# Optimization experiments

Hardware: AMD Instinct MI355X
Metric: run time of the kernel (lower is better)

The kernel has to match this reference:

```python
import jax, jax.numpy as jnp
import numpy as np

HIDDEN = 1024
N_HEAD = 16
HEAD_DIM = HIDDEN // N_HEAD


def setup_inputs() -> dict:
    key = jax.random.key(0)
    ks = jax.random.split(key, 11)
    B, S, D, H, E = 4, 1024, HIDDEN, N_HEAD, HEAD_DIM
    sc = 0.02
    return {
        "query": jax.random.normal(ks[0], (B, S, D), jnp.float32),
        "key": jax.random.normal(ks[1], (B, S, D), jnp.float32),
        "value": jax.random.normal(ks[2], (B, S, D), jnp.float32),
        # per-head projection weights stacked over heads (torch Linear: y = x @ W.T + b)
        "Wq": jax.random.normal(ks[3], (H, D, E), jnp.float32) * sc,
        "bq": jax.random.normal(ks[4], (H, E), jnp.float32) * sc,
        "Wk": jax.random.normal(ks[5], (H, D, E), jnp.float32) * sc,
        "bk": jax.random.normal(ks[6], (H, E), jnp.float32) * sc,
        "Wv": jax.random.normal(ks[7], (H, D, E), jnp.float32) * sc,
        "bv": jax.random.normal(ks[8], (H, E), jnp.float32) * sc,
        "Wo": jax.random.normal(ks[9], (D, D), jnp.float32) * sc,
        "bo": jax.random.normal(ks[10], (D,), jnp.float32) * sc,
    }


def reference(query, key, value, Wq, bq, Wk, bk, Wv, bv, Wo, bo):
    B, S, D = query.shape
    H, _, E = Wq.shape
    # per-head linear projections (vectorized over heads)
    q = jnp.einsum("bsd,hde->bhse", query, Wq) + bq[None, :, None, :]
    k = jnp.einsum("bsd,hde->bhse", key, Wk) + bk[None, :, None, :]
    v = jnp.einsum("bsd,hde->bhse", value, Wv) + bv[None, :, None, :]
    scale = jnp.sqrt(jnp.asarray(E, q.dtype))
    scores = jnp.einsum("bhse,bhte->bhst", q, k) / scale  # [B,H,S,S]
    attn = jax.nn.softmax(scores, axis=-1)  # dropout is identity in eval
    wv = jnp.einsum("bhst,bhte->bhse", attn, v)  # [B,H,S,E]
    # concat heads along feature dim (head h -> slice h*E:(h+1)*E)
    wv = wv.transpose(0, 2, 1, 3).reshape(B, S, H * E)
    out = wv @ Wo.T + bo  # final linear; output dropout identity in eval
    return out
```

## Files before the change

### kernel.cpp

```cpp
#include <hip/hip_runtime.h>

typedef unsigned short u16;
typedef unsigned int u32;
typedef __attribute__((ext_vector_type(8))) short bf16x8;
typedef __attribute__((ext_vector_type(4))) float f32x4;

#define B_SZ 4
#define S_SZ 1024
#define D_SZ 1024
#define H_SZ 16
#define E_SZ 64
#define M_SZ (B_SZ * S_SZ)

__device__ __forceinline__ u16 f2bf(float f) {
  union { float f; unsigned u; } x; x.f = f;
  unsigned r = (x.u + 0x7FFFu + ((x.u >> 16) & 1u)) >> 16;
  return (u16)r;
}

__device__ __forceinline__ u32 pack_bf16(float lo, float hi) {
  return (u32)f2bf(lo) | ((u32)f2bf(hi) << 16);
}

__device__ __forceinline__ void async16(const void* g, void* l) {
  __builtin_amdgcn_global_load_lds(
      (const __attribute__((address_space(1))) void*)g,
      (__attribute__((address_space(3))) void*)l, 16, 0, 0);
}

__device__ __forceinline__ f32x4 mfma16(bf16x8 a, bf16x8 b, f32x4 c) {
  return __builtin_amdgcn_mfma_f32_16x16x32_bf16(a, b, c, 0, 0, 0);
}

__global__ void cast4(const float* __restrict__ q, const float* __restrict__ k,
                      const float* __restrict__ v, const float* __restrict__ Wo,
                      u16* __restrict__ oq, u16* __restrict__ ok,
                      u16* __restrict__ ov, u16* __restrict__ oWo) {
  int gid = blockIdx.x * 256 + threadIdx.x;
  const float* in;
  u16* out;
  int i;
  if (gid < (3 << 19)) {
    int sel = gid >> 19;
    i = (gid & ((1 << 19) - 1)) << 3;
    in = sel == 0 ? q : (sel == 1 ? k : v);
    out = sel == 0 ? oq : (sel == 1 ? ok : ov);
  } else {
    i = (gid - (3 << 19)) << 3;
    in = Wo;
    out = oWo;
  }
  float4 a = *(const float4*)(in + i);
  float4 b = *(const float4*)(in + i + 4);
  alignas(16) u16 r[8];
  r[0] = f2bf(a.x); r[1] = f2bf(a.y); r[2] = f2bf(a.z); r[3] = f2bf(a.w);
  r[4] = f2bf(b.x); r[5] = f2bf(b.y); r[6] = f2bf(b.z); r[7] = f2bf(b.w);
  *(uint4*)(out + i) = *(uint4*)r;
}

__global__ void transW3(const float* __restrict__ Wq, const float* __restrict__ Wk,
                        const float* __restrict__ Wv, u16* __restrict__ Tq,
                        u16* __restrict__ Tk, u16* __restrict__ Tv) {
  __shared__ float tile[64 * 68];
  const int wsel = blockIdx.x >> 8;
  const int bi = blockIdx.x & 255;
  const float* W = wsel == 0 ? Wq : (wsel == 1 ? Wk : Wv);
  u16* WT = wsel == 0 ? Tq : (wsel == 1 ? Tk : Tv);
  const int tid = threadIdx.x;
  const int h = bi >> 4;
  const int d0 = (bi & 15) << 6;
#pragma unroll
  for (int c = 0; c < 4; ++c) {
    const int dd = c * 16 + (tid >> 4);
    const int e4 = (tid & 15) << 2;
    float4 vq = *(const float4*)(W + (h << 16) + ((d0 + dd) << 6) + e4);
    *(float4*)(tile + dd * 68 + e4) = vq;
  }
  __syncthreads();
  {
    const int e = tid >> 2;
    const int dc = (tid & 3) << 4;
    alignas(16) u16 outv[16];
#pragma unroll
    for (int i = 0; i < 16; ++i) outv[i] = f2bf(tile[(dc + i) * 68 + e]);
    u16* dst = WT + (((size_t)(h << 6) + e) << 10) + d0 + dc;
    *(uint4*)(dst) = *(uint4*)outv;
    *(uint4*)(dst + 8) = *(uint4*)(outv + 8);
  }
}

__global__ __launch_bounds__(256)
void gemm3(const u16* __restrict__ qb, const u16* __restrict__ kb, const u16* __restrict__ vb,
           const u16* __restrict__ Tq, const u16* __restrict__ Tk, const u16* __restrict__ Tv,
           const float* __restrict__ bq, const float* __restrict__ bk, const float* __restrict__ bv,
           u16* __restrict__ Qp, u16* __restrict__ Kp, u16* __restrict__ VpT) {
  __shared__ u16 Al[128 * 64];
  __shared__ u16 Bl[128 * 64];
  const int wg = blockIdx.x;
  const int swz = (wg & 7) * 96 + (wg >> 3);
  const int g = swz >> 8;
  const int bi = swz & 255;
  const u16* A = g == 0 ? qb : (g == 1 ? kb : vb);
  const u16* BT = g == 0 ? Tq : (g == 1 ? Tk : Tv);
  const float* bias = g == 0 ? bq : (g == 1 ? bk : bv);
  u16* Cout = g == 0 ? Qp : (g == 1 ? Kp : VpT);
  const float scale = g == 0 ? 0.125f : 1.0f;

  const int tid = threadIdx.x;
  const int wave = tid >> 6;
  const int lane = tid & 63;
  const int l15 = lane & 15, lq = lane >> 4;
  const int bm = bi >> 3;
  const int bn = bi & 7;
  const int row0 = bm << 7, col0 = bn << 7;
  const int wr = ((wave >> 1) & 1) << 6;
  const int wc = (wave & 1) << 6;

  f32x4 acc[4][4];
#pragma unroll
  for (int m = 0; m < 4; ++m)
#pragma unroll
    for (int n = 0; n < 4; ++n) acc[m][n] = (f32x4)0.0f;

  for (int k0 = 0; k0 < 1024; k0 += 64) {
    __syncthreads();
#pragma unroll
    for (int c = 0; c < 4; ++c) {
      const int x = c * 4096 + tid * 16;
      const int gx = x ^ (((x >> 7) & 7) << 4);
      const int row = gx >> 7;
      const int cb = gx & 127;
      const u16* ga = A + (size_t)(row0 + row) * 1024 + k0 + (cb >> 1);
      const u16* gb = BT + (size_t)(col0 + row) * 1024 + k0 + (cb >> 1);
      async16(ga, (char*)Al + x);
      async16(gb, (char*)Bl + x);
    }
    __syncthreads();

    bf16x8 af[4][2], bfr[4][2];
#pragma unroll
    for (int m = 0; m < 4; ++m)
#pragma unroll
      for (int kf = 0; kf < 2; ++kf) {
        int r = wr + m * 16 + l15;
        int byte = ((r << 7) + kf * 64 + lq * 16) ^ ((r & 7) << 4);
        af[m][kf] = *(const bf16x8*)((const char*)Al + byte);
      }
#pragma unroll
    for (int n = 0; n < 4; ++n)
#pragma unroll
      for (int kf = 0; kf < 2; ++kf) {
        int r = wc + n * 16 + l15;
        int byte = ((r << 7) + kf * 64 + lq * 16) ^ ((r & 7) << 4);
        bfr[n][kf] = *(const bf16x8*)((const char*)Bl + byte);
      }
    if (g == 2) {
#pragma unroll
      for (int kf = 0; kf < 2; ++kf)
#pragma unroll
        for (int m = 0; m < 4; ++m)
#pragma unroll
          for (int n = 0; n < 4; ++n)
            acc[m][n] = mfma16(af[m][kf], bfr[n][kf], acc[m][n]);
    } else {
#pragma unroll
      for (int kf = 0; kf < 2; ++kf)
#pragma unroll
        for (int m = 0; m < 4; ++m)
#pragma unroll
          for (int n = 0; n < 4; ++n)
            acc[m][n] = mfma16(bfr[n][kf], af[m][kf], acc[m][n]);
    }
  }

  if (g == 2) {
#pragma unroll
    for (int m = 0; m < 4; ++m)
#pragma unroll
      for (int n = 0; n < 4; ++n) {
        int col = col0 + wc + n * 16 + l15;
        float bv = bias[col];
        int rowb = row0 + wr + m * 16 + lq * 4;
        alignas(8) u16 r4[4];
#pragma unroll
        for (int j = 0; j < 4; ++j) r4[j] = f2bf(acc[m][n][j] + bv);
        *(uint2*)(Cout + (size_t)col * 4096 + rowb) = *(uint2*)r4;
      }
  } else {
    float4 b4[4];
#pragma unroll
    for (int n = 0; n < 4; ++n)
      b4[n] = *(const float4*)(bias + col0 + wc + n * 16 + lq * 4);
#pragma unroll
    for (int m = 0; m < 4; ++m) {
      int row = row0 + wr + m * 16 + l15;
#pragma unroll
      for (int n = 0; n < 4; ++n) {
        int colbase = col0 + wc + n * 16 + lq * 4;
        u32 lo = pack_bf16((acc[m][n][0] + b4[n].x) * scale,
                           (acc[m][n][1] + b4[n].y) * scale);
        u32 hi = pack_bf16((acc[m][n][2] + b4[n].z) * scale,
                           (acc[m][n][3] + b4[n].w) * scale);
        uint2 wv; wv.x = lo; wv.y = hi;
        *(uint2*)(Cout + (size_t)row * 1024 + colbase) = wv;
      }
    }
  }
}

__global__ __launch_bounds__(512)
void gemmO8(const u16* __restrict__ A, const u16* __restrict__ BT,
            const float* __restrict__ bias, float* __restrict__ out) {
  __shared__ u16 Al[128 * 64];
  __shared__ u16 Bl[128 * 64];
  const int tid = threadIdx.x;
  const int wave = tid >> 6;
  const int lane = tid & 63;
  const int l15 = lane & 15, lq = lane >> 4;
  const int wg = blockIdx.x;
  const int bi = (wg & 7) * 32 + (wg >> 3);
  const int bm = bi >> 3;
  const int bn = bi & 7;
  const int row0 = bm << 7, col0 = bn << 7;
  const int wr = (wave >> 1) << 5;
  const int wc = (wave & 1) << 6;

  f32x4 acc[2][4];
#pragma unroll
  for (int m = 0; m < 2; ++m)
#pragma unroll
    for (int n = 0; n < 4; ++n) acc[m][n] = (f32x4)0.0f;

  for (int k0 = 0; k0 < 1024; k0 += 64) {
    __syncthreads();
#pragma unroll
    for (int c = 0; c < 2; ++c) {
      const int x = c * 8192 + tid * 16;
      const int gx = x ^ (((x >> 7) & 7) << 4);
      const int row = gx >> 7;
      const int cb = gx & 127;
      const u16* ga = A + (size_t)(row0 + row) * 1024 + k0 + (cb >> 1);
      const u16* gb = BT + (size_t)(col0 + row) * 1024 + k0 + (cb >> 1);
      async16(ga, (char*)Al + x);
      async16(gb, (char*)Bl + x);
    }
    __syncthreads();

    bf16x8 af[2][2], bfr[4][2];
#pragma unroll
    for (int m = 0; m < 2; ++m)
#pragma unroll
      for (int kf = 0; kf < 2; ++kf) {
        int r = wr + m * 16 + l15;
        int byte = ((r << 7) + kf * 64 + lq * 16) ^ ((r & 7) << 4);
        af[m][kf] = *(const bf16x8*)((const char*)Al + byte);
      }
#pragma unroll
    for (int n = 0; n < 4; ++n)
#pragma unroll
      for (int kf = 0; kf < 2; ++kf) {
        int r = wc + n * 16 + l15;
        int byte = ((r << 7) + kf * 64 + lq * 16) ^ ((r & 7) << 4);
        bfr[n][kf] = *(const bf16x8*)((const char*)Bl + byte);
      }
#pragma unroll
    for (int kf = 0; kf < 2; ++kf)
#pragma unroll
      for (int m = 0; m < 2; ++m)
#pragma unroll
        for (int n = 0; n < 4; ++n)
          acc[m][n] = mfma16(bfr[n][kf], af[m][kf], acc[m][n]);
  }

  float4 b4[4];
#pragma unroll
  for (int n = 0; n < 4; ++n)
    b4[n] = *(const float4*)(bias + col0 + wc + n * 16 + lq * 4);
#pragma unroll
  for (int m = 0; m < 2; ++m) {
    int row = row0 + wr + m * 16 + l15;
#pragma unroll
    for (int n = 0; n < 4; ++n) {
      int colbase = col0 + wc + n * 16 + lq * 4;
      float4 v;
      v.x = acc[m][n][0] + b4[n].x;
      v.y = acc[m][n][1] + b4[n].y;
      v.z = acc[m][n][2] + b4[n].z;
      v.w = acc[m][n][3] + b4[n].w;
      *(float4*)(out + (size_t)row * 1024 + colbase) = v;
    }
  }
}

__global__ __launch_bounds__(256)
void attn(const u16* __restrict__ Qp, const u16* __restrict__ Kp,
          const u16* __restrict__ VpT, u16* __restrict__ Ow) {
  __shared__ alignas(16) u16 Kl[2][64 * 64];
  __shared__ alignas(16) u16 VTl[2][64 * 64];
  __shared__ alignas(16) u16 Pl[4][16 * 64];
  const int tid = threadIdx.x;
  const int wave = tid >> 6;
  const int lane = tid & 63;
  const int l15 = lane & 15, lq = lane >> 4;
  const int wg = blockIdx.x;
  const int swz = (wg & 7) * 128 + (wg >> 3);
  const int qt = swz & 15;
  const int bh = swz >> 4;
  const int b = bh >> 4, h = bh & 15;
  const size_t bS = (size_t)b * S_SZ;

  const int xs0 = tid * 16, xs1 = 4096 + tid * 16;
  const int r0 = xs0 >> 7, r1 = xs1 >> 7;
  const int c0 = ((xs0 & 127) ^ (((xs0 >> 7) & 7) << 4)) >> 1;
  const int c1 = ((xs1 & 127) ^ (((xs1 >> 7) & 7) << 4)) >> 1;
  const u16* Kb0 = Kp + ((bS + r0) << 10) + h * 64 + c0;
  const u16* Kb1 = Kp + ((bS + r1) << 10) + h * 64 + c1;
  const u16* Vb0 = VpT + (size_t)(h * 64 + r0) * 4096 + bS + c0;
  const u16* Vb1 = VpT + (size_t)(h * 64 + r1) * 4096 + bS + c1;

  bf16x8 aq[2];
  {
    const u16* qptr = Qp + ((bS + qt * 64 + wave * 16 + l15) << 10) + h * 64 + lq * 8;
    aq[0] = *(const bf16x8*)(qptr);
    aq[1] = *(const bf16x8*)(qptr + 32);
  }

  f32x4 o[4];
#pragma unroll
  for (int n = 0; n < 4; ++n) o[n] = (f32x4)0.0f;
  float m_run = -1e30f;
  float l_run = 0.f;
  u16* Pw = Pl[wave];

  async16(Kb0, (char*)Kl[0] + xs0);
  async16(Kb1, (char*)Kl[0] + xs1);
  async16(Vb0, (char*)VTl[0] + xs0);
  async16(Vb1, (char*)VTl[0] + xs1);
  __syncthreads();

  int buf = 0;
  for (int t0 = 0; t0 < S_SZ; t0 += 64) {
    if (t0 + 64 < S_SZ) {
      const int tn = t0 + 64;
      async16(Kb0 + ((size_t)tn << 10), (char*)Kl[buf ^ 1] + xs0);
      async16(Kb1 + ((size_t)tn << 10), (char*)Kl[buf ^ 1] + xs1);
      async16(Vb0 + tn, (char*)VTl[buf ^ 1] + xs0);
      async16(Vb1 + tn, (char*)VTl[buf ^ 1] + xs1);
    }

    f32x4 s[4];
#pragma unroll
    for (int n = 0; n < 4; ++n) s[n] = (f32x4)0.0f;
    __builtin_amdgcn_s_setprio(1);
#pragma unroll
    for (int n = 0; n < 4; ++n)
#pragma unroll
      for (int kf = 0; kf < 2; ++kf) {
        int r = n * 16 + l15;
        int byte = ((r << 7) + kf * 64 + lq * 16) ^ ((r & 7) << 4);
        bf16x8 bk = *(const bf16x8*)((const char*)Kl[buf] + byte);
        s[n] = mfma16(bk, aq[kf], s[n]);
      }
    __builtin_amdgcn_s_setprio(0);

    float mx = s[0][0];
#pragma unroll
    for (int n = 0; n < 4; ++n)
#pragma unroll
      for (int j = 0; j < 4; ++j) mx = fmaxf(mx, s[n][j]);
    mx = fmaxf(mx, __shfl_xor(mx, 16, 64));
    mx = fmaxf(mx, __shfl_xor(mx, 32, 64));

    if (__any(mx > m_run + 8.0f)) {
      float mn = fmaxf(m_run, mx);
      float alpha = __expf(m_run - mn);
      m_run = mn;
      l_run *= alpha;
      float a0 = __shfl(alpha, lq * 4 + 0, 64);
      float a1 = __shfl(alpha, lq * 4 + 1, 64);
      float a2 = __shfl(alpha, lq * 4 + 2, 64);
      float a3 = __shfl(alpha, lq * 4 + 3, 64);
#pragma unroll
      for (int n = 0; n < 4; ++n) {
        o[n][0] *= a0; o[n][1] *= a1; o[n][2] *= a2; o[n][3] *= a3;
      }
    }

    float rs = 0.f;
#pragma unroll
    for (int n = 0; n < 4; ++n) {
      float p0 = __expf(s[n][0] - m_run);
      float p1 = __expf(s[n][1] - m_run);
      float p2 = __expf(s[n][2] - m_run);
      float p3 = __expf(s[n][3] - m_run);
      rs += (p0 + p1) + (p2 + p3);
      u32 lo = pack_bf16(p0, p1);
      u32 hi = pack_bf16(p2, p3);
      int byte = (l15 << 7) + (((n * 32 + lq * 8)) ^ ((l15 & 7) << 4));
      uint2 wv; wv.x = lo; wv.y = hi;
      *(uint2*)((char*)Pw + byte) = wv;
    }
    rs += __shfl_xor(rs, 16, 64);
    rs += __shfl_xor(rs, 32, 64);
    l_run += rs;

    __builtin_amdgcn_s_setprio(1);
#pragma unroll
    for (int kf = 0; kf < 2; ++kf) {
      int pbyte = (l15 << 7) + ((kf * 64 + lq * 16) ^ ((l15 & 7) << 4));
      bf16x8 pa = *(const bf16x8*)((const char*)Pw + pbyte);
#pragma unroll
      for (int n = 0; n < 4; ++n) {
        int vr = n * 16 + l15;
        int byte = ((vr << 7) + kf * 64 + lq * 16) ^ ((vr & 7) << 4);
        bf16x8 bv = *(const bf16x8*)((const char*)VTl[buf] + byte);
        o[n] = mfma16(pa, bv, o[n]);
      }
    }
    __builtin_amdgcn_s_setprio(0);

    __syncthreads();
    buf ^= 1;
  }

  float li0 = __shfl(l_run, lq * 4 + 0, 64);
  float li1 = __shfl(l_run, lq * 4 + 1, 64);
  float li2 = __shfl(l_run, lq * 4 + 2, 64);
  float li3 = __shfl(l_run, lq * 4 + 3, 64);
  float inv0 = 1.0f / li0, inv1 = 1.0f / li1, inv2 = 1.0f / li2, inv3 = 1.0f / li3;
#pragma unroll
  for (int n = 0; n < 4; ++n) {
    float vals[4] = {o[n][0] * inv0, o[n][1] * inv1, o[n][2] * inv2, o[n][3] * inv3};
#pragma unroll
    for (int j = 0; j < 4; ++j) {
      int row = qt * 64 + wave * 16 + lq * 4 + j;
      int col = h * 64 + n * 16 + l15;
      Ow[((bS + row) << 10) + col] = f2bf(vals[j]);
    }
  }
}

extern "C" void kernel_launch(void* const* d_in, const int* in_sizes, int n_in,
                              void* d_out, int out_size, void* d_ws, size_t ws_size,
                              hipStream_t stream) {
  const float* q  = (const float*)d_in[0];
  const float* k  = (const float*)d_in[1];
  const float* v  = (const float*)d_in[2];
  const float* Wq = (const float*)d_in[3];
  const float* bq = (const float*)d_in[4];
  const float* Wk = (const float*)d_in[5];
  const float* bk = (const float*)d_in[6];
  const float* Wv = (const float*)d_in[7];
  const float* bv = (const float*)d_in[8];
  const float* Wo = (const float*)d_in[9];
  const float* bo = (const float*)d_in[10];

  char* w = (char*)d_ws;
  const size_t MB = 1u << 20;
  u16* qb  = (u16*)(w + 0 * MB);
  u16* kb  = (u16*)(w + 8 * MB);
  u16* vb  = (u16*)(w + 16 * MB);
  u16* WqT = (u16*)(w + 24 * MB);
  u16* WkT = (u16*)(w + 26 * MB);
  u16* WvT = (u16*)(w + 28 * MB);
  u16* Wob = (u16*)(w + 30 * MB);
  u16* Qp  = (u16*)(w + 32 * MB);
  u16* Kp  = (u16*)(w + 40 * MB);
  u16* VpT = (u16*)(w + 48 * MB);
  u16* wvb = (u16*)(w + 56 * MB);

  cast4<<<6656, 256, 0, stream>>>(q, k, v, Wo, qb, kb, vb, Wob);
  transW3<<<768, 256, 0, stream>>>(Wq, Wk, Wv, WqT, WkT, WvT);

  gemm3<<<768, 256, 0, stream>>>(qb, kb, vb, WqT, WkT, WvT, bq, bk, bv, Qp, Kp, VpT);

  attn<<<B_SZ * H_SZ * (S_SZ / 64), 256, 0, stream>>>(Qp, Kp, VpT, wvb);

  gemmO8<<<256, 512, 0, stream>>>(wvb, Wob, bo, (float*)d_out);
}
```

Before: 122.4 us.

## Double-buffer LDS tiles in projection GEMMs and widen gemm3 to 512 threads

Both the QKV projection GEMM and the output GEMM now use two LDS buffers per operand. The next K-slice is prefetched before computing the current one, and only one barrier is issued per iteration instead of two. gemm3 also goes from 4 to 8 waves per block, each wave owning a 32x64 sub-tile, to raise wave-level parallelism. The risks are that the 4-blocks-per-CU launch bound can force register limits low enough to spill, and that the doubled LDS footprint lowers how many blocks fit per CU.

Measured after the change: 128.9 us. 5.3% more time.

```diff
diff --git a/kernel.cpp b/kernel.cpp
--- a/kernel.cpp
+++ b/kernel.cpp
@@ -89,13 +89,13 @@
   }
 }
 
-__global__ __launch_bounds__(256)
+__global__ __launch_bounds__(512, 4)
 void gemm3(const u16* __restrict__ qb, const u16* __restrict__ kb, const u16* __restrict__ vb,
            const u16* __restrict__ Tq, const u16* __restrict__ Tk, const u16* __restrict__ Tv,
            const float* __restrict__ bq, const float* __restrict__ bk, const float* __restrict__ bv,
            u16* __restrict__ Qp, u16* __restrict__ Kp, u16* __restrict__ VpT) {
-  __shared__ u16 Al[128 * 64];
-  __shared__ u16 Bl[128 * 64];
+  __shared__ u16 Al[2][128 * 64];
+  __shared__ u16 Bl[2][128 * 64];
   const int wg = blockIdx.x;
   const int swz = (wg & 7) * 96 + (wg >> 3);
   const int g = swz >> 8;
@@ -113,38 +113,51 @@
   const int bm = bi >> 3;
   const int bn = bi & 7;
   const int row0 = bm << 7, col0 = bn << 7;
-  const int wr = ((wave >> 1) & 1) << 6;
+  const int wr = (wave >> 1) << 5;
   const int wc = (wave & 1) << 6;
 
-  f32x4 acc[4][4];
-#pragma unroll
-  for (int m = 0; m < 4; ++m)
+  int xs[2], rowS[2], cbS[2];
+#pragma unroll
+  for (int c = 0; c < 2; ++c) {
+    int x = c * 8192 + tid * 16;
+    int gx = x ^ (((x >> 7) & 7) << 4);
+    xs[c] = x;
+    rowS[c] = gx >> 7;
+    cbS[c] = (gx & 127) >> 1;
+  }
+
+  f32x4 acc[2][4];
+#pragma unroll
+  for (int m = 0; m < 2; ++m)
 #pragma unroll
     for (int n = 0; n < 4; ++n) acc[m][n] = (f32x4)0.0f;
 
+#pragma unroll
+  for (int c = 0; c < 2; ++c) {
+    async16(A + (size_t)(row0 + rowS[c]) * 1024 + cbS[c], (char*)Al[0] + xs[c]);
+    async16(BT + (size_t)(col0 + rowS[c]) * 1024 + cbS[c], (char*)Bl[0] + xs[c]);
+  }
+  __syncthreads();
+
+  int buf = 0;
   for (int k0 = 0; k0 < 1024; k0 += 64) {
-    __syncthreads();
-#pragma unroll
-    for (int c = 0; c < 4; ++c) {
-      const int x = c * 4096 + tid * 16;
-      const int gx = x ^ (((x >> 7) & 7) << 4);
-      const int row = gx >> 7;
-      const int cb = gx & 127;
-      const u16* ga = A + (size_t)(row0 + row) * 1024 + k0 + (cb >> 1);
-      const u16* gb = BT + (size_t)(col0 + row) * 1024 + k0 + (cb >> 1);
-      async16(ga, (char*)Al + x);
-      async16(gb, (char*)Bl + x);
-    }
-    __syncthreads();
-
-    bf16x8 af[4][2], bfr[4][2];
-#pragma unroll
-    for (int m = 0; m < 4; ++m)
+    if (k0 + 64 < 1024) {
+      const int kn = k0 + 64;
+#pragma unroll
+      for (int c = 0; c < 2; ++c) {
+        async16(A + (size_t)(row0 + rowS[c]) * 1024 + kn + cbS[c], (char*)Al[buf ^ 1] + xs[c]);
+        async16(BT + (size_t)(col0 + rowS[c]) * 1024 + kn + cbS[c], (char*)Bl[buf ^ 1] + xs[c]);
+      }
+    }
+
+    bf16x8 af[2][2], bfr[4][2];
+#pragma unroll
+    for (int m = 0; m < 2; ++m)
 #pragma unroll
       for (int kf = 0; kf < 2; ++kf) {
         int r = wr + m * 16 + l15;
         int byte = ((r << 7) + kf * 64 + lq * 16) ^ ((r & 7) << 4);
-        af[m][kf] = *(const bf16x8*)((const char*)Al + byte);
+        af[m][kf] = *(const bf16x8*)((const char*)Al[buf] + byte);
       }
 #pragma unroll
     for (int n = 0; n < 4; ++n)
@@ -152,13 +165,13 @@
       for (int kf = 0; kf < 2; ++kf) {
         int r = wc + n * 16 + l15;
         int byte = ((r << 7) + kf * 64 + lq * 16) ^ ((r & 7) << 4);
-        bfr[n][kf] = *(const bf16x8*)((const char*)Bl + byte);
+        bfr[n][kf] = *(const bf16x8*)((const char*)Bl[buf] + byte);
       }
     if (g == 2) {
 #pragma unroll
       for (int kf = 0; kf < 2; ++kf)
 #pragma unroll
-        for (int m = 0; m < 4; ++m)
+        for (int m = 0; m < 2; ++m)
 #pragma unroll
           for (int n = 0; n < 4; ++n)
             acc[m][n] = mfma16(af[m][kf], bfr[n][kf], acc[m][n]);
@@ -166,16 +179,19 @@
 #pragma unroll
       for (int kf = 0; kf < 2; ++kf)
 #pragma unroll
-        for (int m = 0; m < 4; ++m)
+        for (int m = 0; m < 2; ++m)
 #pragma unroll
           for (int n = 0; n < 4; ++n)
             acc[m][n] = mfma16(bfr[n][kf], af[m][kf], acc[m][n]);
     }
+
+    __syncthreads();
+    buf ^= 1;
   }
 
   if (g == 2) {
 #pragma unroll
-    for (int m = 0; m < 4; ++m)
+    for (int m = 0; m < 2; ++m)
 #pragma unroll
       for (int n = 0; n < 4; ++n) {
         int col = col0 + wc + n * 16 + l15;
@@ -192,7 +208,7 @@
     for (int n = 0; n < 4; ++n)
       b4[n] = *(const float4*)(bias + col0 + wc + n * 16 + lq * 4);
 #pragma unroll
-    for (int m = 0; m < 4; ++m) {
+    for (int m = 0; m < 2; ++m) {
       int row = row0 + wr + m * 16 + l15;
 #pragma unroll
       for (int n = 0; n < 4; ++n) {
@@ -208,11 +224,11 @@
   }
 }
 
-__global__ __launch_bounds__(512)
+__global__ __launch_bounds__(512, 4)
 void gemmO8(const u16* __restrict__ A, const u16* __restrict__ BT,
             const float* __restrict__ bias, float* __restrict__ out) {
-  __shared__ u16 Al[128 * 64];
-  __shared__ u16 Bl[128 * 64];
+  __shared__ u16 Al[2][128 * 64];
+  __shared__ u16 Bl[2][128 * 64];
   const int tid = threadIdx.x;
   const int wave = tid >> 6;
   const int lane = tid & 63;
@@ -225,26 +241,39 @@
   const int wr = (wave >> 1) << 5;
   const int wc = (wave & 1) << 6;
 
+  int xs[2], rowS[2], cbS[2];
+#pragma unroll
+  for (int c = 0; c < 2; ++c) {
+    int x = c * 8192 + tid * 16;
+    int gx = x ^ (((x >> 7) & 7) << 4);
+    xs[c] = x;
+    rowS[c] = gx >> 7;
+    cbS[c] = (gx & 127) >> 1;
+  }
+
   f32x4 acc[2][4];
 #pragma unroll
   for (int m = 0; m < 2; ++m)
 #pragma unroll
     for (int n = 0; n < 4; ++n) acc[m][n] = (f32x4)0.0f;
 
+#pragma unroll
+  for (int c = 0; c < 2; ++c) {
+    async16(A + (size_t)(row0 + rowS[c]) * 1024 + cbS[c], (char*)Al[0] + xs[c]);
+    async16(BT + (size_t)(col0 + rowS[c]) * 1024 + cbS[c], (char*)Bl[0] + xs[c]);
+  }
+  __syncthreads();
+
+  int buf = 0;
   for (int k0 = 0; k0 < 1024; k0 += 64) {
-    __syncthreads();
-#pragma unroll
-    for (int c = 0; c < 2; ++c) {
-      const int x = c * 8192 + tid * 16;
-      const int gx = x ^ (((x >> 7) & 7) << 4);
-      const int row = gx >> 7;
-      const int cb = gx & 127;
-      const u16* ga = A + (size_t)(row0 + row) * 1024 + k0 + (cb >> 1);
-      const u16* gb = BT + (size_t)(col0 + row) * 1024 + k0 + (cb >> 1);
-      async16(ga, (char*)Al + x);
-      async16(gb, (char*)Bl + x);
-    }
-    __syncthreads();
+    if (k0 + 64 < 1024) {
+      const int kn = k0 + 64;
+#pragma unroll
+      for (int c = 0; c < 2; ++c) {
+        async16(A + (size_t)(row0 + rowS[c]) * 1024 + kn + cbS[c], (char*)Al[buf ^ 1] + xs[c]);
+        async16(BT + (size_t)(col0 + rowS[c]) * 1024 + kn + cbS[c], (char*)Bl[buf ^ 1] + xs[c]);
+      }
+    }
 
     bf16x8 af[2][2], bfr[4][2];
 #pragma unroll
@@ -253,7 +282,7 @@
       for (int kf = 0; kf < 2; ++kf) {
         int r = wr + m * 16 + l15;
         int byte = ((r << 7) + kf * 64 + lq * 16) ^ ((r & 7) << 4);
-        af[m][kf] = *(const bf16x8*)((const char*)Al + byte);
+        af[m][kf] = *(const bf16x8*)((const char*)Al[buf] + byte);
       }
 #pragma unroll
     for (int n = 0; n < 4; ++n)
@@ -261,7 +290,7 @@
       for (int kf = 0; kf < 2; ++kf) {
         int r = wc + n * 16 + l15;
         int byte = ((r << 7) + kf * 64 + lq * 16) ^ ((r & 7) << 4);
-        bfr[n][kf] = *(const bf16x8*)((const char*)Bl + byte);
+        bfr[n][kf] = *(const bf16x8*)((const char*)Bl[buf] + byte);
       }
 #pragma unroll
     for (int kf = 0; kf < 2; ++kf)
@@ -270,6 +299,9 @@
 #pragma unroll
         for (int n = 0; n < 4; ++n)
           acc[m][n] = mfma16(bfr[n][kf], af[m][kf], acc[m][n]);
+
+    __syncthreads();
+    buf ^= 1;
   }
 
   float4 b4[4];
@@ -472,7 +504,7 @@
   cast4<<<6656, 256, 0, stream>>>(q, k, v, Wo, qb, kb, vb, Wob);
   transW3<<<768, 256, 0, stream>>>(Wq, Wk, Wv, WqT, WkT, WvT);
 
-  gemm3<<<768, 256, 0, stream>>>(qb, kb, vb, WqT, WkT, WvT, bq, bk, bv, Qp, Kp, VpT);
+  gemm3<<<768, 512, 0, stream>>>(qb, kb, vb, WqT, WkT, WvT, bq, bk, bv, Qp, Kp, VpT);
 
   attn<<<B_SZ * H_SZ * (S_SZ / 64), 256, 0, stream>>>(Qp, Kp, VpT, wvb);
 
```
